# Kernel optimization log

Hardware: AMD Instinct MI355X
Metric: run time of the kernel (lower is better)

## Reference

```python
import jax, jax.numpy as jnp
import numpy as np

D_MODEL = 1024
NHEAD = 16
HEAD_DIM = D_MODEL // NHEAD  # 64
THETA = 10000.0


def apply_rope(t):
    # t: [B, H, S, D]. Interleaved-pair RoPE (lucidrains rotary-embedding-torch
    # rotate_queries_or_keys), positions = arange(S), theta = 10000.
    B, H, S, D = t.shape
    inv_freq = 1.0 / (THETA ** (jnp.arange(0, D, 2, dtype=jnp.float32) / D))  # [D/2]
    ang = jnp.arange(S, dtype=jnp.float32)[:, None] * inv_freq               # [S, D/2]
    cos = jnp.cos(ang).astype(t.dtype)
    sin = jnp.sin(ang).astype(t.dtype)
    tp = t.reshape(B, H, S, D // 2, 2)
    x1, x2 = tp[..., 0], tp[..., 1]
    rot = jnp.stack([x1 * cos - x2 * sin, x1 * sin + x2 * cos], axis=-1)
    return rot.reshape(B, H, S, D)


def setup_inputs() -> dict:
    key = jax.random.key(0)
    k0, k1, k2, k3, k4 = jax.random.split(key, 5)
    B, Sx, Sc = 2, 2048, 2048
    sc = 0.02  # weight init scale
    return {
        "x": jax.random.normal(k0, (B, Sx, D_MODEL), jnp.float32),
        "context": jax.random.normal(k1, (B, Sc, D_MODEL), jnp.float32),
        "Wq": jax.random.normal(k2, (D_MODEL, D_MODEL), jnp.float32) * sc,
        "Wv": jax.random.normal(k3, (D_MODEL, D_MODEL), jnp.float32) * sc,
        "Wo": jax.random.normal(k4, (D_MODEL, D_MODEL), jnp.float32) * sc,
        "bo": jnp.zeros((D_MODEL,), jnp.float32),
        "x_pos": jnp.arange(B * Sx, dtype=jnp.int64).reshape(B, Sx) % Sx,
        "context_pos": jnp.arange(B * Sc, dtype=jnp.int64).reshape(B, Sc) % Sc,
    }


def reference(x, context, Wq, Wv, Wo, bo, x_pos, context_pos):
    # x_pos/context_pos are unused when both streams use the internal
    # RotaryEmbedding (is_imu1=is_imu2=True), matching the original forward.
    B, Sx, _ = x.shape
    Sc = context.shape[1]
    q = (x @ Wq.T).reshape(B, Sx, NHEAD, HEAD_DIM).transpose(0, 2, 1, 3)
    # NOTE: original code uses projq (not projk) for keys — replicated here.
    k = (context @ Wq.T).reshape(B, Sc, NHEAD, HEAD_DIM).transpose(0, 2, 1, 3)
    v = (context @ Wv.T).reshape(B, Sc, NHEAD, HEAD_DIM).transpose(0, 2, 1, 3)
    q = apply_rope(q)
    k = apply_rope(k)
    scale = 1.0 / jnp.sqrt(jnp.asarray(HEAD_DIM, q.dtype))
    attn = jax.nn.softmax(jnp.einsum("bhqd,bhkd->bhqk", q, k) * scale, axis=-1)
    out = jnp.einsum("bhqk,bhkd->bhqd", attn, v)            # [B,H,Sx,hd]
    out = out.transpose(0, 2, 1, 3).reshape(B, Sx, D_MODEL)  # [B,Sx,d_model]
    return out @ Wo.T + bo
```

## Files before the change

kernel.cpp:

```cpp
#include <hip/hip_runtime.h>
#include <cmath>


typedef __bf16 bf16x8 __attribute__((ext_vector_type(8)));
typedef __bf16 bf16x4 __attribute__((ext_vector_type(4)));
typedef float f32x4 __attribute__((ext_vector_type(4)));
typedef float f32x16 __attribute__((ext_vector_type(16)));
typedef unsigned u32x4v __attribute__((ext_vector_type(4)));

#define MFMA(A, B, C) __builtin_amdgcn_mfma_f32_16x16x32_bf16(A, B, C, 0, 0, 0)
#define MFMA32(A, B, C) __builtin_amdgcn_mfma_f32_32x32x16_bf16(A, B, C, 0, 0, 0)
#define GLL16(g, l)                                                        \
  __builtin_amdgcn_global_load_lds(                                        \
      (const __attribute__((address_space(1))) unsigned int*)(g),          \
      (__attribute__((address_space(3))) unsigned int*)(l), 16, 0, 0)

#define VMCNT(N) asm volatile("s_waitcnt vmcnt(" #N ")" ::: "memory")
#define BARM() asm volatile("s_barrier" ::: "memory")
#define LGKM0() asm volatile("s_waitcnt lgkmcnt(0)" ::: "memory")

__global__ __launch_bounds__(256) void cvt_all_kernel(
    const float* __restrict__ x, const float* __restrict__ ctx,
    const float* __restrict__ Wq, const float* __restrict__ Wv,
    const float* __restrict__ Wo, __bf16* __restrict__ xb, __bf16* __restrict__ cb,
    __bf16* __restrict__ Wqb, __bf16* __restrict__ Wvb, __bf16* __restrict__ Wob) {
  int base = blockIdx.x * 512 + threadIdx.x;
  const float* src;
  __bf16* dst;
  int off;
  if (base < 1048576) { src = x; dst = xb; off = 0; }
  else if (base < 2097152) { src = ctx; dst = cb; off = 1048576; }
  else if (base < 2359296) { src = Wq; dst = Wqb; off = 2097152; }
  else if (base < 2621440) { src = Wv; dst = Wvb; off = 2359296; }
  else { src = Wo; dst = Wob; off = 2621440; }
#pragma unroll
  for (int jj = 0; jj < 2; jj++) {
    int j = base - off + jj * 256;
    float4 f = ((const float4*)src)[j];
    bf16x4 o;
    o[0] = (__bf16)f.x; o[1] = (__bf16)f.y; o[2] = (__bf16)f.z; o[3] = (__bf16)f.w;
    ((bf16x4*)dst)[j] = o;
  }
}

__global__ __launch_bounds__(512, 2) void gemm_proj(const __bf16* __restrict__ A0,
                                                    const __bf16* __restrict__ W0,
                                                    void* __restrict__ outQ,
                                                    void* __restrict__ outK,
                                                    void* __restrict__ outV) {
  const int tid = threadIdx.x;
  const int wave = tid >> 6, lane = tid & 63, quad = lane >> 4, l15 = lane & 15;
  const int wm = wave >> 2, wn = wave & 3;

  const int id = blockIdx.x;
  int m0, n0;
  const __bf16* A;
  const __bf16* W;
  bool vmode;
  if (id < 128) {
    const int xcd = id & 7, j = id >> 3;
    m0 = (xcd * 4 + (j & 3)) * 256;
    n0 = (j >> 2) * 256;
    A = A0;
    W = W0;
    vmode = false;
  } else {
    const int vid = id - 128;
    const int xcd = vid & 7, j = vid >> 3;
    m0 = (xcd * 2 + (j & 1)) * 256;
    n0 = (j >> 1) * 256;
    A = A0 + (size_t)4096 * 1024;
    W = W0 + (size_t)1024 * 1024;
    vmode = true;
  }

  __shared__ __attribute__((aligned(16))) __bf16 As[2][2][8192];
  __shared__ __attribute__((aligned(16))) __bf16 Bs[2][2][8192];

  const int srow = tid >> 2;
  const int kcg = (tid & 3) ^ (srow & 3);
  const size_t aoff0 = (size_t)srow * 1024 + kcg * 8;
  const size_t aoff1 = (size_t)(srow + 128) * 1024 + kcg * 8;
  const __bf16* Ag = A + (size_t)m0 * 1024;
  const __bf16* Wg = W + (size_t)n0 * 1024;
  const int ldst0 = wave * 512;
  const int ldst1 = 4096 + wave * 512;

  auto stageA = [&](int slot, int kh, int kel) {
    GLL16(Ag + aoff0 + kel, &As[slot][kh][ldst0]);
    GLL16(Ag + aoff1 + kel, &As[slot][kh][ldst1]);
  };
  auto stageB = [&](int slot, int kh, int kel) {
    GLL16(Wg + aoff0 + kel, &Bs[slot][kh][ldst0]);
    GLL16(Wg + aoff1 + kel, &Bs[slot][kh][ldst1]);
  };

  const int xk = (quad ^ (l15 & 3)) * 8;
  int afo[8], bfo[4];
#pragma unroll
  for (int mf = 0; mf < 8; mf++) afo[mf] = (wm * 128 + mf * 16 + l15) * 32 + xk;
#pragma unroll
  for (int nf = 0; nf < 4; nf++) bfo[nf] = (wn * 64 + nf * 16 + l15) * 32 + xk;

  f32x4 acc[8][4] = {};
  bf16x8 bf[4], af[4];

  auto loadB = [&](int slot, int kh) {
#pragma unroll
    for (int nf = 0; nf < 4; nf++) bf[nf] = *(const bf16x8*)&Bs[slot][kh][bfo[nf]];
  };
  auto loadA = [&](int slot, int kh, int mfg) {
#pragma unroll
    for (int mf = 0; mf < 4; mf++)
      af[mf] = *(const bf16x8*)&As[slot][kh][afo[mfg * 4 + mf]];
  };
  auto mfma16 = [&](int mfg) {
    __builtin_amdgcn_s_setprio(1);
#pragma unroll
    for (int mf = 0; mf < 4; mf++)
#pragma unroll
      for (int nf = 0; nf < 4; nf++)
        acc[mfg * 4 + mf][nf] = MFMA(af[mf], bf[nf], acc[mfg * 4 + mf][nf]);
    __builtin_amdgcn_s_setprio(0);
  };

  stageA(0, 0, 0);  stageB(0, 0, 0);
  stageA(0, 1, 32); stageB(0, 1, 32);
  stageA(1, 0, 64); stageB(1, 0, 64);
  VMCNT(8); BARM();

#pragma unroll 1
  for (int j = 0; j < 7; j++) {
    const int kb = j * 128;
    loadB(0, 0); loadA(0, 0, 0); stageA(1, 1, kb + 96);
    BARM(); LGKM0(); mfma16(0); BARM();
    loadA(0, 0, 1); stageB(1, 1, kb + 96);
    BARM(); LGKM0(); mfma16(1); VMCNT(8); BARM();
    loadB(0, 1); loadA(0, 1, 0); stageA(0, 0, kb + 128);
    BARM(); LGKM0(); mfma16(0); BARM();
    loadA(0, 1, 1); stageB(0, 0, kb + 128);
    BARM(); LGKM0(); mfma16(1); VMCNT(8); BARM();
    loadB(1, 0); loadA(1, 0, 0); stageA(0, 1, kb + 160);
    BARM(); LGKM0(); mfma16(0); BARM();
    loadA(1, 0, 1); stageB(0, 1, kb + 160);
    BARM(); LGKM0(); mfma16(1); VMCNT(8); BARM();
    loadB(1, 1); loadA(1, 1, 0); stageA(1, 0, kb + 192);
    BARM(); LGKM0(); mfma16(0); BARM();
    loadA(1, 1, 1); stageB(1, 0, kb + 192);
    BARM(); LGKM0(); mfma16(1); VMCNT(8); BARM();
  }
  {
    loadB(0, 0); loadA(0, 0, 0); stageA(1, 1, 992);
    BARM(); LGKM0(); mfma16(0); BARM();
    loadA(0, 0, 1); stageB(1, 1, 992);
    BARM(); LGKM0(); mfma16(1); VMCNT(8); BARM();
    loadB(0, 1); loadA(0, 1, 0);
    BARM(); LGKM0(); mfma16(0); BARM();
    loadA(0, 1, 1);
    BARM(); LGKM0(); mfma16(1); VMCNT(4); BARM();
    loadB(1, 0); loadA(1, 0, 0);
    BARM(); LGKM0(); mfma16(0); BARM();
    loadA(1, 0, 1);
    BARM(); LGKM0(); mfma16(1); VMCNT(0); BARM();
    loadB(1, 1); loadA(1, 1, 0);
    BARM(); LGKM0(); mfma16(0); BARM();
    loadA(1, 1, 1);
    BARM(); LGKM0(); mfma16(1);
  }

  if (!vmode) {
    const int isK = (m0 >= 4096);
    __bf16* O = (__bf16*)(isK ? outK : outQ);
    const float qsc = isK ? 1.0f : 0.18033688f;
    const int mb = m0 & 4095;
#pragma unroll
    for (int nf = 0; nf < 4; nf++) {
      const int n = n0 + wn * 64 + nf * 16 + l15;
      const int h = n >> 6, d = n & 63, p = d >> 1;
      const float invf_rev =
          __builtin_amdgcn_exp2f(-((float)p * 0.41524101f + 2.6514961f));
#pragma unroll
      for (int mf = 0; mf < 8; mf++) {
#pragma unroll
        for (int r = 0; r < 4; r++) {
          const int row = mb + wm * 128 + mf * 16 + quad * 4 + r;
          const int s = row & 2047, b = row >> 11;
          float v = acc[mf][nf][r];
          float pv = __shfl_xor(v, 1, 64);
          float fr = __builtin_amdgcn_fractf((float)s * invf_rev);
          float sn = __builtin_amdgcn_sinf(fr);
          float cs = __builtin_amdgcn_cosf(fr);
          float res = (lane & 1) ? (pv * sn + v * cs) : (v * cs - pv * sn);
          O[((size_t)(b * 16 + h) * 2048 + s) * 64 + d] = (__bf16)(res * qsc);
        }
      }
    }
  } else {
    __bf16* O = (__bf16*)outV;
#pragma unroll
    for (int nf = 0; nf < 4; nf++) {
      const int n = n0 + wn * 64 + nf * 16 + l15;
      const int h = n >> 6, d = n & 63;
#pragma unroll
      for (int mf = 0; mf < 8; mf++) {
        const int rowb = m0 + wm * 128 + mf * 16 + quad * 4;
        const int s = rowb & 2047, b = rowb >> 11;
        bf16x4 o;
#pragma unroll
        for (int r = 0; r < 4; r++) o[r] = (__bf16)acc[mf][nf][r];
        *(bf16x4*)(O + ((size_t)(b * 16 + h) * 64 + d) * 2048 + s) = o;
      }
    }
  }
}

__global__ __launch_bounds__(256) void gemm_out(const __bf16* __restrict__ A,
                                                const __bf16* __restrict__ W,
                                                float* __restrict__ O,
                                                const float* __restrict__ bias) {
  const int tid = threadIdx.x;
  const int wave = tid >> 6, lane = tid & 63, quad = lane >> 4, l15 = lane & 15;
  const int mw = wave >> 1, nw = wave & 1;
  const int id = blockIdx.x;
  const int xcd = id & 7, j = id >> 3;
  const int m0 = (xcd * 4 + (j & 3)) * 128;
  const int n0 = (j >> 2) * 64;

  __shared__ __attribute__((aligned(16))) __bf16 As[3][4096];
  __shared__ __attribute__((aligned(16))) __bf16 Ws[3][2048];

  int goff[2];
#pragma unroll
  for (int jj = 0; jj < 2; jj++) {
    const int s = jj * 256 + tid;
    const int row = s >> 2;
    const int kcg = (s & 3) ^ ((row >> 1) & 3);
    goff[jj] = row * 1024 + kcg * 8;
  }
  const int wrow = tid >> 2;
  const int wkcg = (tid & 3) ^ ((wrow >> 1) & 3);
  const int goffw = wrow * 1024 + wkcg * 8;

  const __bf16* Ag = A + (size_t)m0 * 1024;
  const __bf16* Wg = W + (size_t)n0 * 1024;
  const int ldsoff0 = wave * 512;
  const int ldsoff1 = 2048 + wave * 512;

  const int sw = (l15 >> 1) & 3;
  int afoff[4], wfoff[2];
#pragma unroll
  for (int t = 0; t < 4; t++)
    afoff[t] = (mw * 64 + t * 16 + l15) * 32 + (quad ^ sw) * 8;
#pragma unroll
  for (int t = 0; t < 2; t++)
    wfoff[t] = (nw * 32 + t * 16 + l15) * 32 + (quad ^ sw) * 8;

  f32x4 acc[4][2] = {};

  auto stage = [&](int buf, int k0) {
    GLL16(Ag + goff[0] + k0, &As[buf][ldsoff0]);
    GLL16(Ag + goff[1] + k0, &As[buf][ldsoff1]);
    GLL16(Wg + goffw + k0, &Ws[buf][ldsoff0]);
  };
  auto compute = [&](int buf) {
    bf16x8 af[4], wf[2];
#pragma unroll
    for (int t = 0; t < 4; t++) af[t] = *(const bf16x8*)&As[buf][afoff[t]];
#pragma unroll
    for (int t = 0; t < 2; t++) wf[t] = *(const bf16x8*)&Ws[buf][wfoff[t]];
#pragma unroll
    for (int mt = 0; mt < 4; mt++)
#pragma unroll
      for (int nt = 0; nt < 2; nt++) acc[mt][nt] = MFMA(af[mt], wf[nt], acc[mt][nt]);
  };

  stage(0, 0);
  stage(1, 32);
  int buf = 0;
  for (int c = 0; c < 32; c++) {
    __syncthreads();
    if (c + 2 < 32) {
      int nb = buf + 2;
      if (nb >= 3) nb -= 3;
      stage(nb, (c + 2) * 32);
    }
    compute(buf);
    buf = (buf == 2) ? 0 : buf + 1;
  }

#pragma unroll
  for (int nt = 0; nt < 2; nt++) {
    const int n = n0 + nw * 32 + nt * 16 + l15;
    const float bv = bias[n];
#pragma unroll
    for (int mt = 0; mt < 4; mt++) {
#pragma unroll
      for (int r = 0; r < 4; r++) {
        const int row = m0 + mw * 64 + mt * 16 + quad * 4 + r;
        O[(size_t)row * 1024 + n] = acc[mt][nt][r] + bv;
      }
    }
  }
}

__global__ __launch_bounds__(512, 4) void attn_kernel(const __bf16* __restrict__ Q,
                                                      const __bf16* __restrict__ K,
                                                      const __bf16* __restrict__ Vt,
                                                      __bf16* __restrict__ Aout) {
  const int tid = threadIdx.x;
  const int wave = tid >> 6, lane = tid & 63;
  const int l31 = lane & 31, hi = lane >> 5;
  const int qg = wave >> 1, kg = wave & 1;
  const int id = blockIdx.x;
  const int j = id >> 3;
  const int bh = ((id & 7) << 2) | (j & 3);
  const int q0 = (j >> 2) << 7;

  const __bf16* Qb = Q + (size_t)bh * (2048 * 64);
  const __bf16* Kb = K + (size_t)bh * (2048 * 64);
  const __bf16* Vb = Vt + (size_t)bh * (64 * 2048);

  __shared__ __attribute__((aligned(16))) __bf16 Kbuf[4][4096];
  __shared__ __attribute__((aligned(16))) __bf16 Vbuf[4][4096];

  bf16x8 qf[4];
  {
    const __bf16* qp = Qb + (size_t)(q0 + qg * 32 + l31) * 64 + hi * 8;
#pragma unroll
    for (int i = 0; i < 4; i++) qf[i] = *(const bf16x8*)(qp + i * 16);
  }

  const int s0 = wave * 64 + lane;
  const int r0 = s0 >> 3, c0 = (s0 & 7) ^ (r0 & 7);
  const __bf16* kgp = Kb + r0 * 64 + c0 * 8;
  const __bf16* vgp = Vb + r0 * 2048 + c0 * 8;
  const int klds = wave * 512;

  int koff[4];
  {
    const int rk = kg * 32 + l31;
#pragma unroll
    for (int i = 0; i < 4; i++) koff[i] = rk * 64 + (((2 * i + hi) ^ (rk & 7)) * 8);
  }
  int voff[2][2];
#pragma unroll
  for (int dt = 0; dt < 2; dt++) {
    const int rv = dt * 32 + l31;
#pragma unroll
    for (int ks = 0; ks < 2; ks++)
      voff[dt][ks] = rv * 64 + (((kg * 4 + ks * 2 + hi) ^ (rv & 7)) * 8);
  }

  f32x4 rs4 = {};
  f32x16 oacc[2] = {};

  auto stage = [&](int buf, int kt) {
    GLL16(kgp + kt * 64, &Kbuf[buf][klds]);
    GLL16(vgp + kt, &Vbuf[buf][klds]);
  };

  auto compute = [&](int buf) {
    f32x16 s = {};
#pragma unroll
    for (int i = 0; i < 4; i++) {
      bf16x8 kf = *(const bf16x8*)&Kbuf[buf][koff[i]];
      s = MFMA32(kf, qf[i], s);
    }
    float pe[16];
#pragma unroll
    for (int r = 0; r < 16; r++) pe[r] = __builtin_amdgcn_exp2f(s[r]);
#pragma unroll
    for (int r = 0; r < 16; r++) rs4[r & 3] += pe[r];
    bf16x8 pa[2];
#pragma unroll
    for (int sl = 0; sl < 2; sl++) {
      unsigned wa, wb, wc, wd;
      asm("v_cvt_pk_bf16_f32 %0, %1, %2" : "=v"(wa) : "v"(pe[8 * sl + 0]), "v"(pe[8 * sl + 1]));
      asm("v_cvt_pk_bf16_f32 %0, %1, %2" : "=v"(wb) : "v"(pe[8 * sl + 4]), "v"(pe[8 * sl + 5]));
      asm("v_cvt_pk_bf16_f32 %0, %1, %2" : "=v"(wc) : "v"(pe[8 * sl + 2]), "v"(pe[8 * sl + 3]));
      asm("v_cvt_pk_bf16_f32 %0, %1, %2" : "=v"(wd) : "v"(pe[8 * sl + 6]), "v"(pe[8 * sl + 7]));
      asm("v_permlane32_swap_b32 %0, %1" : "+v"(wa), "+v"(wb));
      asm("v_permlane32_swap_b32 %0, %1" : "+v"(wc), "+v"(wd));
      u32x4v t;
      t[0] = wa; t[1] = wc; t[2] = wb; t[3] = wd;
      pa[sl] = __builtin_bit_cast(bf16x8, t);
    }
#pragma unroll
    for (int dt = 0; dt < 2; dt++)
#pragma unroll
      for (int ks = 0; ks < 2; ks++) {
        bf16x8 vf = *(const bf16x8*)&Vbuf[buf][voff[dt][ks]];
        oacc[dt] = MFMA32(pa[ks], vf, oacc[dt]);
      }
  };

  stage(0, 0);
  stage(1, 64);
  for (int kt = 0; kt < 2048; kt += 128) {
    const int p = (kt >> 7) & 1;
    __syncthreads();
    if (kt + 128 < 2048) {
      stage(2 * (p ^ 1), kt + 128);
      stage(2 * (p ^ 1) + 1, kt + 192);
    }
    compute(2 * p);
    compute(2 * p + 1);
  }

  __syncthreads();
  float* Ored = (float*)&Kbuf[0][0];
  float* Lred = (float*)&Vbuf[0][0];

  float lw = (rs4[0] + rs4[1]) + (rs4[2] + rs4[3]);
  lw += __shfl_xor(lw, 32, 64);
  Lred[wave * 64 + lane] = lw;
  if (kg == 1) {
#pragma unroll
    for (int dt = 0; dt < 2; dt++)
#pragma unroll
      for (int r = 0; r < 16; r++)
        Ored[(qg * 32 + dt * 16 + r) * 64 + lane] = oacc[dt][r];
  }
  __syncthreads();
  if (kg == 0) {
    const int b = bh >> 4, h = bh & 15;
#pragma unroll
    for (int r = 0; r < 16; r++) {
      const int qrow = (r & 3) + 8 * (r >> 2) + 4 * hi;
      const float lt =
          Lred[(qg * 2) * 64 + qrow] + Lred[(qg * 2 + 1) * 64 + qrow];
      const float inv = 1.f / lt;
      const int qAbs = q0 + qg * 32 + qrow;
#pragma unroll
      for (int dt = 0; dt < 2; dt++) {
        const float o = oacc[dt][r] + Ored[(qg * 32 + dt * 16 + r) * 64 + lane];
        Aout[((size_t)(b * 2048 + qAbs)) * 1024 + h * 64 + dt * 32 + l31] =
            (__bf16)(o * inv);
      }
    }
  }
}

extern "C" void kernel_launch(void* const* d_in, const int* in_sizes, int n_in,
                              void* d_out, int out_size, void* d_ws, size_t ws_size,
                              hipStream_t stream) {
  const float* x   = (const float*)d_in[0];
  const float* ctx = (const float*)d_in[1];
  const float* Wq  = (const float*)d_in[2];
  const float* Wv  = (const float*)d_in[3];
  const float* Wo  = (const float*)d_in[4];
  const float* bo  = (const float*)d_in[5];

  char* ws = (char*)d_ws;
  const size_t MB = 1024 * 1024;
  __bf16* xb   = (__bf16*)(ws + 0 * MB);
  __bf16* cb   = (__bf16*)(ws + 8 * MB);
  __bf16* Wqb  = (__bf16*)(ws + 16 * MB);
  __bf16* Wvb  = (__bf16*)(ws + 18 * MB);
  __bf16* Wob  = (__bf16*)(ws + 20 * MB);
  __bf16* qh   = (__bf16*)(ws + 22 * MB);
  __bf16* kh   = (__bf16*)(ws + 30 * MB);
  __bf16* vt   = (__bf16*)(ws + 38 * MB);
  __bf16* attn = xb;

  cvt_all_kernel<<<5632, 256, 0, stream>>>(x, ctx, Wq, Wv, Wo, xb, cb, Wqb, Wvb, Wob);

  gemm_proj<<<192, 512, 0, stream>>>(xb, Wqb, (void*)qh, (void*)kh, (void*)vt);

  attn_kernel<<<512, 512, 0, stream>>>(qh, kh, vt, attn);

  gemm_out<<<512, 256, 0, stream>>>(attn, Wob, (float*)d_out, bo);
}
```

Baseline: 201.6 us.

## Rewrite output GEMM with 256x128 tiles and interleaved barrier-scheduled pipeline

```diff
diff --git a/kernel.cpp b/kernel.cpp
--- a/kernel.cpp
+++ b/kernel.cpp
@@ -214,90 +214,121 @@
   }
 }
 
-__global__ __launch_bounds__(256) void gemm_out(const __bf16* __restrict__ A,
-                                                const __bf16* __restrict__ W,
-                                                float* __restrict__ O,
-                                                const float* __restrict__ bias) {
+__global__ __launch_bounds__(512, 2) void gemm_out(const __bf16* __restrict__ A,
+                                                   const __bf16* __restrict__ W,
+                                                   float* __restrict__ O,
+                                                   const float* __restrict__ bias) {
   const int tid = threadIdx.x;
   const int wave = tid >> 6, lane = tid & 63, quad = lane >> 4, l15 = lane & 15;
-  const int mw = wave >> 1, nw = wave & 1;
+  const int wm = wave >> 1, wn = wave & 1;
   const int id = blockIdx.x;
-  const int xcd = id & 7, j = id >> 3;
-  const int m0 = (xcd * 4 + (j & 3)) * 128;
-  const int n0 = (j >> 2) * 64;
-
-  __shared__ __attribute__((aligned(16))) __bf16 As[3][4096];
-  __shared__ __attribute__((aligned(16))) __bf16 Ws[3][2048];
-
-  int goff[2];
-#pragma unroll
-  for (int jj = 0; jj < 2; jj++) {
-    const int s = jj * 256 + tid;
-    const int row = s >> 2;
-    const int kcg = (s & 3) ^ ((row >> 1) & 3);
-    goff[jj] = row * 1024 + kcg * 8;
-  }
-  const int wrow = tid >> 2;
-  const int wkcg = (tid & 3) ^ ((wrow >> 1) & 3);
-  const int goffw = wrow * 1024 + wkcg * 8;
-
+  const int xcd = id & 7, jj = id >> 3;
+  const int m0 = (xcd * 2 + (jj & 1)) * 256;
+  const int n0 = (jj >> 1) * 128;
+
+  __shared__ __attribute__((aligned(16))) __bf16 As[2][2][8192];
+  __shared__ __attribute__((aligned(16))) __bf16 Bs[2][2][4096];
+
+  const int srow = tid >> 2;
+  const int kcg = (tid & 3) ^ (srow & 3);
+  const size_t aoff0 = (size_t)srow * 1024 + kcg * 8;
+  const size_t aoff1 = (size_t)(srow + 128) * 1024 + kcg * 8;
   const __bf16* Ag = A + (size_t)m0 * 1024;
   const __bf16* Wg = W + (size_t)n0 * 1024;
-  const int ldsoff0 = wave * 512;
-  const int ldsoff1 = 2048 + wave * 512;
-
-  const int sw = (l15 >> 1) & 3;
-  int afoff[4], wfoff[2];
-#pragma unroll
-  for (int t = 0; t < 4; t++)
-    afoff[t] = (mw * 64 + t * 16 + l15) * 32 + (quad ^ sw) * 8;
-#pragma unroll
-  for (int t = 0; t < 2; t++)
-    wfoff[t] = (nw * 32 + t * 16 + l15) * 32 + (quad ^ sw) * 8;
-
-  f32x4 acc[4][2] = {};
-
-  auto stage = [&](int buf, int k0) {
-    GLL16(Ag + goff[0] + k0, &As[buf][ldsoff0]);
-    GLL16(Ag + goff[1] + k0, &As[buf][ldsoff1]);
-    GLL16(Wg + goffw + k0, &Ws[buf][ldsoff0]);
-  };
-  auto compute = [&](int buf) {
-    bf16x8 af[4], wf[2];
-#pragma unroll
-    for (int t = 0; t < 4; t++) af[t] = *(const bf16x8*)&As[buf][afoff[t]];
-#pragma unroll
-    for (int t = 0; t < 2; t++) wf[t] = *(const bf16x8*)&Ws[buf][wfoff[t]];
-#pragma unroll
-    for (int mt = 0; mt < 4; mt++)
-#pragma unroll
-      for (int nt = 0; nt < 2; nt++) acc[mt][nt] = MFMA(af[mt], wf[nt], acc[mt][nt]);
-  };
-
-  stage(0, 0);
-  stage(1, 32);
-  int buf = 0;
-  for (int c = 0; c < 32; c++) {
-    __syncthreads();
-    if (c + 2 < 32) {
-      int nb = buf + 2;
-      if (nb >= 3) nb -= 3;
-      stage(nb, (c + 2) * 32);
-    }
-    compute(buf);
-    buf = (buf == 2) ? 0 : buf + 1;
-  }
-
-#pragma unroll
-  for (int nt = 0; nt < 2; nt++) {
-    const int n = n0 + nw * 32 + nt * 16 + l15;
+  const int ldst0 = wave * 512;
+  const int ldst1 = 4096 + wave * 512;
+
+  auto stageA = [&](int slot, int kh, int kel) {
+    GLL16(Ag + aoff0 + kel, &As[slot][kh][ldst0]);
+    GLL16(Ag + aoff1 + kel, &As[slot][kh][ldst1]);
+  };
+  auto stageB = [&](int slot, int kh, int kel) {
+    GLL16(Wg + aoff0 + kel, &Bs[slot][kh][ldst0]);
+  };
+
+  const int xk = (quad ^ (l15 & 3)) * 8;
+  int afo[4], bfo[4];
+#pragma unroll
+  for (int mf = 0; mf < 4; mf++) afo[mf] = (wm * 64 + mf * 16 + l15) * 32 + xk;
+#pragma unroll
+  for (int nf = 0; nf < 4; nf++) bfo[nf] = (wn * 64 + nf * 16 + l15) * 32 + xk;
+
+  f32x4 acc[4][4] = {};
+  bf16x8 bf[4], af[2];
+
+  auto loadB = [&](int slot, int kh) {
+#pragma unroll
+    for (int nf = 0; nf < 4; nf++) bf[nf] = *(const bf16x8*)&Bs[slot][kh][bfo[nf]];
+  };
+  auto loadA = [&](int slot, int kh, int mfg) {
+#pragma unroll
+    for (int mf = 0; mf < 2; mf++)
+      af[mf] = *(const bf16x8*)&As[slot][kh][afo[mfg * 2 + mf]];
+  };
+  auto mfma8 = [&](int mfg) {
+    __builtin_amdgcn_s_setprio(1);
+#pragma unroll
+    for (int mf = 0; mf < 2; mf++)
+#pragma unroll
+      for (int nf = 0; nf < 4; nf++)
+        acc[mfg * 2 + mf][nf] = MFMA(af[mf], bf[nf], acc[mfg * 2 + mf][nf]);
+    __builtin_amdgcn_s_setprio(0);
+  };
+
+  stageA(0, 0, 0);  stageB(0, 0, 0);
+  stageA(0, 1, 32); stageB(0, 1, 32);
+  stageA(1, 0, 64); stageB(1, 0, 64);
+  VMCNT(6); BARM();
+
+#pragma unroll 1
+  for (int j = 0; j < 7; j++) {
+    const int kb = j * 128;
+    loadB(0, 0); loadA(0, 0, 0); stageA(1, 1, kb + 96);
+    BARM(); LGKM0(); mfma8(0); BARM();
+    loadA(0, 0, 1); stageB(1, 1, kb + 96);
+    BARM(); LGKM0(); mfma8(1); VMCNT(6); BARM();
+    loadB(0, 1); loadA(0, 1, 0); stageA(0, 0, kb + 128);
+    BARM(); LGKM0(); mfma8(0); BARM();
+    loadA(0, 1, 1); stageB(0, 0, kb + 128);
+    BARM(); LGKM0(); mfma8(1); VMCNT(6); BARM();
+    loadB(1, 0); loadA(1, 0, 0); stageA(0, 1, kb + 160);
+    BARM(); LGKM0(); mfma8(0); BARM();
+    loadA(1, 0, 1); stageB(0, 1, kb + 160);
+    BARM(); LGKM0(); mfma8(1); VMCNT(6); BARM();
+    loadB(1, 1); loadA(1, 1, 0); stageA(1, 0, kb + 192);
+    BARM(); LGKM0(); mfma8(0); BARM();
+    loadA(1, 1, 1); stageB(1, 0, kb + 192);
+    BARM(); LGKM0(); mfma8(1); VMCNT(6); BARM();
+  }
+  {
+    loadB(0, 0); loadA(0, 0, 0); stageA(1, 1, 992);
+    BARM(); LGKM0(); mfma8(0); BARM();
+    loadA(0, 0, 1); stageB(1, 1, 992);
+    BARM(); LGKM0(); mfma8(1); VMCNT(6); BARM();
+    loadB(0, 1); loadA(0, 1, 0);
+    BARM(); LGKM0(); mfma8(0); BARM();
+    loadA(0, 1, 1);
+    BARM(); LGKM0(); mfma8(1); VMCNT(3); BARM();
+    loadB(1, 0); loadA(1, 0, 0);
+    BARM(); LGKM0(); mfma8(0); BARM();
+    loadA(1, 0, 1);
+    BARM(); LGKM0(); mfma8(1); VMCNT(0); BARM();
+    loadB(1, 1); loadA(1, 1, 0);
+    BARM(); LGKM0(); mfma8(0); BARM();
+    loadA(1, 1, 1);
+    BARM(); LGKM0(); mfma8(1);
+  }
+
+#pragma unroll
+  for (int nf = 0; nf < 4; nf++) {
+    const int n = n0 + wn * 64 + nf * 16 + l15;
     const float bv = bias[n];
 #pragma unroll
-    for (int mt = 0; mt < 4; mt++) {
+    for (int mf = 0; mf < 4; mf++) {
 #pragma unroll
       for (int r = 0; r < 4; r++) {
-        const int row = m0 + mw * 64 + mt * 16 + quad * 4 + r;
-        O[(size_t)row * 1024 + n] = acc[mt][nt][r] + bv;
+        const int row = m0 + wm * 64 + mf * 16 + quad * 4 + r;
+        O[(size_t)row * 1024 + n] = acc[mf][nf][r] + bv;
       }
     }
   }
@@ -469,5 +500,5 @@
 
   attn_kernel<<<512, 512, 0, stream>>>(qh, kh, vt, attn);
 
-  gemm_out<<<512, 256, 0, stream>>>(attn, Wob, (float*)d_out, bo);
+  gemm_out<<<128, 512, 0, stream>>>(attn, Wob, (float*)d_out, bo);
 }
```

Result: no change. 201.1 us (-0.2%).
